# Optimization experiments

Measured on AMD Instinct MI355X. Metric: run time of the kernel, lower is better.

Reference implementation:

```python
import jax, jax.numpy as jnp
import numpy as np

H = 128
IN = 2048
PROJ = 64
EPS = 1e-5


def setup_inputs() -> dict:
    key = jax.random.key(0)
    ks = jax.random.split(key, 12)
    B, T = 64, 512
    s_in = 1.0 / np.sqrt(H)  # torch RNN init: U(-1/sqrt(H), 1/sqrt(H))
    u = lambda k, shape, s: jax.random.uniform(k, shape, jnp.float32, -s, s)
    return {
        "x": jax.random.normal(ks[0], (B, T, IN), jnp.float32),
        "W_ih1": u(ks[1], (H, IN), s_in),
        "W_hh1": u(ks[2], (H, H), s_in),
        "b_ih1": u(ks[3], (H,), s_in),
        "b_hh1": u(ks[4], (H,), s_in),
        "W_ih2": u(ks[5], (H, H), s_in),
        "W_hh2": u(ks[6], (H, H), s_in),
        "b_ih2": u(ks[7], (H,), s_in),
        "b_hh2": u(ks[8], (H,), s_in),
        "W_proj": u(ks[9], (PROJ, H), 1.0 / np.sqrt(H)),
        "b_proj": u(ks[10], (PROJ,), 1.0 / np.sqrt(H)),
        "gamma": jnp.ones((PROJ,), jnp.float32),
        "beta": jnp.zeros((PROJ,), jnp.float32),
    }


def _rnn(xproj, W_hh, collect):
    # xproj: [B, T, H] = x @ W_ih^T + b_ih + b_hh (biases folded in)
    B = xproj.shape[0]
    h0 = jnp.zeros((B, H), xproj.dtype)
    xs = jnp.swapaxes(xproj, 0, 1)  # [T, B, H]

    def step(h, xp):
        h = jnp.tanh(xp + h @ W_hh.T)
        return h, (h if collect else None)

    h_last, ys = jax.lax.scan(step, h0, xs)
    return h_last, (jnp.swapaxes(ys, 0, 1) if collect else None)


def reference(x, W_ih1, W_hh1, b_ih1, b_hh1, W_ih2, W_hh2, b_ih2, b_hh2,
              W_proj, b_proj, gamma, beta):
    # layer 1: hoist the big input GEMM out of the recurrence
    xp1 = jnp.einsum("bti,hi->bth", x, W_ih1) + (b_ih1 + b_hh1)
    _, y1 = _rnn(xp1, W_hh1, collect=True)  # [B, T, H]
    # layer 2: only final hidden state is needed
    xp2 = jnp.einsum("bth,gh->btg", y1, W_ih2) + (b_ih2 + b_hh2)
    h2, _ = _rnn(xp2, W_hh2, collect=False)  # [B, H]
    # projection + LayerNorm
    z = h2 @ W_proj.T + b_proj  # [B, 64]
    mu = jnp.mean(z, axis=-1, keepdims=True)
    var = jnp.mean((z - mu) ** 2, axis=-1, keepdims=True)
    return (z - mu) * jax.lax.rsqrt(var + EPS) * gamma + beta
```

## Files before the change

kernel.cpp:

```cpp
#include <hip/hip_runtime.h>
#include <math.h>

#define H 128
#define IN 2048
#define PROJ 64
#define BT 32768
#define T_STEPS 512
#define BATCH 64
#define BM 128
#define BKA 64

using f32x4  = __attribute__((ext_vector_type(4))) float;
using bfrag  = __attribute__((ext_vector_type(8))) short;
using h2_t   = __attribute__((ext_vector_type(2))) _Float16;

__device__ __forceinline__ unsigned cvtpk(float lo, float hi) {
  unsigned r;
  asm("v_cvt_pk_bf16_f32 %0, %1, %2" : "=v"(r) : "v"(lo), "v"(hi));
  return r;
}

__global__ __launch_bounds__(512) void xp1_gemm(
    const float* __restrict__ x, const float* __restrict__ W,
    const float* __restrict__ b1, const float* __restrict__ b2,
    float* __restrict__ xp1) {
  __shared__ __align__(16) char As[2][BM * BKA * 2];
  __shared__ __align__(16) char Bs[2][H * BKA * 2];
  const int t  = threadIdx.x;
  const int m0 = blockIdx.x * BM;
  const int wv = t >> 6, l = t & 63;
  const int wm = wv >> 2;
  const int wn = wv & 3;
  const int lr = l & 15;
  const int lq = l >> 4;

  const float* xg[4];
  const float* wg[4];
  int so[4];
#pragma unroll
  for (int i = 0; i < 4; ++i) {
    int c = t + 512 * i, r = c >> 4, k4 = c & 15;
    xg[i] = x + (size_t)(m0 + r) * IN + k4 * 4;
    wg[i] = W + (size_t)r * IN + k4 * 4;
    so[i] = (r * 128 + k4 * 8) ^ ((r & 7) << 4);
  }
  int ao[2][4], bo[2][2];
#pragma unroll
  for (int kf = 0; kf < 2; ++kf) {
#pragma unroll
    for (int mf = 0; mf < 4; ++mf) {
      int r = wm * 64 + mf * 16 + lr;
      ao[kf][mf] = (r * 128 + kf * 64 + lq * 16) ^ ((r & 7) << 4);
    }
#pragma unroll
    for (int nf = 0; nf < 2; ++nf) {
      int r = wn * 32 + nf * 16 + lr;
      bo[kf][nf] = (r * 128 + kf * 64 + lq * 16) ^ ((r & 7) << 4);
    }
  }

  f32x4 acc[4][2];
#pragma unroll
  for (int mf = 0; mf < 4; ++mf)
#pragma unroll
    for (int nf = 0; nf < 2; ++nf)
#pragma unroll
      for (int j = 0; j < 4; ++j) acc[mf][nf][j] = 0.f;

  float4 xr[4], wr[4];
#pragma unroll
  for (int i = 0; i < 4; ++i) {
    xr[i] = *(const float4*)&xg[i][0];
    wr[i] = *(const float4*)&wg[i][0];
  }
#pragma unroll
  for (int i = 0; i < 4; ++i) {
    uint2 ux; ux.x = cvtpk(xr[i].x, xr[i].y); ux.y = cvtpk(xr[i].z, xr[i].w);
    *(uint2*)(As[0] + so[i]) = ux;
    uint2 uw; uw.x = cvtpk(wr[i].x, wr[i].y); uw.y = cvtpk(wr[i].z, wr[i].w);
    *(uint2*)(Bs[0] + so[i]) = uw;
  }
  __syncthreads();

  for (int tc = 0; tc < 32; ++tc) {
    const int kc = (tc + 1) * BKA;
    if (tc < 31) {
#pragma unroll
      for (int i = 0; i < 4; ++i) {
        xr[i] = *(const float4*)&xg[i][kc];
        wr[i] = *(const float4*)&wg[i][kc];
      }
    }
    const char* Ab = As[tc & 1];
    const char* Bb = Bs[tc & 1];
#pragma unroll
    for (int kf = 0; kf < 2; ++kf) {
      bfrag af[4], bf[2];
#pragma unroll
      for (int mf = 0; mf < 4; ++mf) af[mf] = *(const bfrag*)(Ab + ao[kf][mf]);
#pragma unroll
      for (int nf = 0; nf < 2; ++nf) bf[nf] = *(const bfrag*)(Bb + bo[kf][nf]);
#pragma unroll
      for (int mf = 0; mf < 4; ++mf)
#pragma unroll
        for (int nf = 0; nf < 2; ++nf)
          acc[mf][nf] = __builtin_amdgcn_mfma_f32_16x16x32_bf16(
              af[mf], bf[nf], acc[mf][nf], 0, 0, 0);
    }
    if (tc < 31) {
      char* Aw = As[(tc + 1) & 1];
      char* Bw = Bs[(tc + 1) & 1];
#pragma unroll
      for (int i = 0; i < 4; ++i) {
        uint2 ux; ux.x = cvtpk(xr[i].x, xr[i].y); ux.y = cvtpk(xr[i].z, xr[i].w);
        *(uint2*)(Aw + so[i]) = ux;
        uint2 uw; uw.x = cvtpk(wr[i].x, wr[i].y); uw.y = cvtpk(wr[i].z, wr[i].w);
        *(uint2*)(Bw + so[i]) = uw;
      }
    }
    __syncthreads();
  }

#pragma unroll
  for (int nf = 0; nf < 2; ++nf) {
    int n = wn * 32 + nf * 16 + lr;
    float bias = b1[n] + b2[n];
#pragma unroll
    for (int mf = 0; mf < 4; ++mf) {
      int mr = m0 + wm * 64 + mf * 16 + lq * 4;
#pragma unroll
      for (int j = 0; j < 4; ++j)
        xp1[(size_t)(mr + j) * H + n] = acc[mf][nf][j] + bias;
    }
  }
}

struct Wrow { unsigned p0, p1, p2, p3, p4, p5, p6, p7; };

__device__ __forceinline__ float4 gload16(const float* p) {
  float4 r;
  asm volatile("global_load_dwordx4 %0, %1, off" : "=v"(r) : "v"(p));
  return r;
}

__device__ __forceinline__ unsigned pkh(float x, float y) {
  h2_t p = {(_Float16)x, (_Float16)y};
  return __builtin_bit_cast(unsigned, p);
}

__device__ __forceinline__ Wrow packrow(float4 a, float4 b, float4 c,
                                        float4 d) {
  Wrow w = {pkh(a.x, a.y), pkh(a.z, a.w), pkh(b.x, b.y), pkh(b.z, b.w),
            pkh(c.x, c.y), pkh(c.z, c.w), pkh(d.x, d.y), pkh(d.z, d.w)};
  return w;
}

__device__ __forceinline__ float d2(unsigned w, int h, float acc) {
  return __builtin_amdgcn_fdot2(__builtin_bit_cast(h2_t, w),
                                __builtin_bit_cast(h2_t, (unsigned)h), acc,
                                false);
}

__device__ __forceinline__ float dot16(Wrow w, int4 lo, int4 hi, float acc) {
  acc = d2(w.p0, lo.x, acc);
  acc = d2(w.p1, lo.y, acc);
  acc = d2(w.p2, lo.z, acc);
  acc = d2(w.p3, lo.w, acc);
  acc = d2(w.p4, hi.x, acc);
  acc = d2(w.p5, hi.y, acc);
  acc = d2(w.p6, hi.z, acc);
  acc = d2(w.p7, hi.w, acc);
  return acc;
}

template <int CTRL>
__device__ __forceinline__ float dpp_add(float x) {
  return x + __builtin_bit_cast(
                 float, __builtin_amdgcn_mov_dpp(__builtin_bit_cast(int, x),
                                                 CTRL, 0xf, 0xf, true));
}

__device__ __forceinline__ float red8(float v) {
  v = dpp_add<0xB1>(v);
  v = dpp_add<0x4E>(v);
  v = dpp_add<0x141>(v);
  return v;
}

__device__ __forceinline__ float fast_tanh(float x) {
  float e = __expf(2.0f * x);
  return 1.0f - 2.0f / (e + 1.0f);
}

__global__ __launch_bounds__(512)
__attribute__((amdgpu_waves_per_eu(1, 2)))
void rnn_fused(
    const float* __restrict__ xp1,
    const float* __restrict__ W_hh1, const float* __restrict__ W_ih2,
    const float* __restrict__ W_hh2, const float* __restrict__ b_ih2,
    const float* __restrict__ b_hh2, const float* __restrict__ W_proj,
    const float* __restrict__ b_proj, const float* __restrict__ gamma,
    const float* __restrict__ beta, float* __restrict__ out) {
  __shared__ __align__(16) _Float16 h1s[2][H];
  __shared__ __align__(16) _Float16 h2s[2][H];
  const int t = threadIdx.x;
  const int b = blockIdx.x;
  const int l = t & 63;
  const int w = t >> 6;
  const int g = (l >> 3) & 7;
  const int q = l & 7;
  const int r0 = 16 * w + g;
  const int r1 = r0 + 8;

  const float* pA = &W_hh1[r0 * H + 16 * q];
  const float* pB = &W_hh1[r1 * H + 16 * q];
  const float* pC = &W_ih2[r0 * H + 16 * q];
  const float* pD = &W_ih2[r1 * H + 16 * q];
  const float* pE = &W_hh2[r0 * H + 16 * q];
  const float* pF = &W_hh2[r1 * H + 16 * q];
  float4 A0 = gload16(pA), A1 = gload16(pA + 4), A2 = gload16(pA + 8), A3 = gload16(pA + 12);
  float4 B0 = gload16(pB), B1 = gload16(pB + 4), B2 = gload16(pB + 8), B3 = gload16(pB + 12);
  float4 C0 = gload16(pC), C1 = gload16(pC + 4), C2 = gload16(pC + 8), C3 = gload16(pC + 12);
  float4 D0 = gload16(pD), D1 = gload16(pD + 4), D2 = gload16(pD + 8), D3 = gload16(pD + 12);
  float4 E0 = gload16(pE), E1 = gload16(pE + 4), E2 = gload16(pE + 8), E3 = gload16(pE + 12);
  float4 F0 = gload16(pF), F1 = gload16(pF + 4), F2 = gload16(pF + 8), F3 = gload16(pF + 12);
  asm volatile("s_waitcnt vmcnt(0)" ::: "memory");

  Wrow W1r0 = packrow(A0, A1, A2, A3);
  Wrow W1r1 = packrow(B0, B1, B2, B3);
  Wrow W2r0 = packrow(C0, C1, C2, C3);
  Wrow W2r1 = packrow(D0, D1, D2, D3);
  Wrow W3r0 = packrow(E0, E1, E2, E3);
  Wrow W3r1 = packrow(F0, F1, F2, F3);

  const float bias2_0 = b_ih2[r0] + b_hh2[r0];
  const float bias2_1 = b_ih2[r1] + b_hh2[r1];

  if (t < H) { h1s[1][t] = (_Float16)0.f; h2s[1][t] = (_Float16)0.f; }
  __syncthreads();

  const float* xpr0 = xp1 + (size_t)b * T_STEPS * H + r0;
  const float* xpr1 = xpr0 + 8;

  if (q == 0) {
    h1s[0][r0] = (_Float16)fast_tanh(xpr0[0]);
    h1s[0][r1] = (_Float16)fast_tanh(xpr1[0]);
  }
  __syncthreads();

  float xpc0 = xpr0[H];
  float xpc1 = xpr1[H];

  for (int i = 1; i < T_STEPS; ++i) {
    const _Float16* h1p = h1s[(i - 1) & 1];
    const _Float16* h2p = h2s[i & 1];
    _Float16* h1w = h1s[i & 1];
    _Float16* h2w = h2s[(i - 1) & 1];

    float nx0 = 0.f, nx1 = 0.f;
    if (i + 1 < T_STEPS) {
      nx0 = xpr0[(size_t)(i + 1) * H];
      nx1 = xpr1[(size_t)(i + 1) * H];
    }

    int4 l1 = *(const int4*)&h1p[16 * q];
    int4 u1 = *(const int4*)&h1p[16 * q + 8];
    int4 l2 = *(const int4*)&h2p[16 * q];
    int4 u2 = *(const int4*)&h2p[16 * q + 8];

    float a0 = dot16(W1r0, l1, u1, 0.f);
    float a1 = dot16(W1r1, l1, u1, 0.f);
    float c0 = dot16(W3r0, l2, u2, 0.f);
    float c1 = dot16(W3r1, l2, u2, 0.f);
    float bb0 = dot16(W2r0, l1, u1, c0);
    float bb1 = dot16(W2r1, l1, u1, c1);

    a0 = red8(a0); a1 = red8(a1);
    bb0 = red8(bb0); bb1 = red8(bb1);

    float h1n0 = fast_tanh(xpc0 + a0);
    float h1n1 = fast_tanh(xpc1 + a1);
    float h2n0 = fast_tanh(bias2_0 + bb0);
    float h2n1 = fast_tanh(bias2_1 + bb1);
    if (q == 0) {
      h1w[r0] = (_Float16)h1n0; h1w[r1] = (_Float16)h1n1;
      h2w[r0] = (_Float16)h2n0; h2w[r1] = (_Float16)h2n1;
    }
    __syncthreads();
    xpc0 = nx0; xpc1 = nx1;
  }

  {
    const _Float16* h1p = h1s[(T_STEPS - 1) & 1];
    const _Float16* h2p = h2s[T_STEPS & 1];
    _Float16* h2w = h2s[(T_STEPS - 1) & 1];
    int4 l1 = *(const int4*)&h1p[16 * q];
    int4 u1 = *(const int4*)&h1p[16 * q + 8];
    int4 l2 = *(const int4*)&h2p[16 * q];
    int4 u2 = *(const int4*)&h2p[16 * q + 8];
    float c0 = dot16(W3r0, l2, u2, 0.f);
    float c1 = dot16(W3r1, l2, u2, 0.f);
    float bb0 = dot16(W2r0, l1, u1, c0);
    float bb1 = dot16(W2r1, l1, u1, c1);
    bb0 = red8(bb0); bb1 = red8(bb1);
    if (q == 0) {
      h2w[r0] = (_Float16)fast_tanh(bias2_0 + bb0);
      h2w[r1] = (_Float16)fast_tanh(bias2_1 + bb1);
    }
    __syncthreads();
  }

  if (t < PROJ) {
    const float* wp = W_proj + t * H;
    float z = b_proj[t];
#pragma unroll
    for (int i = 0; i < 32; ++i) {
      float4 wv = *(const float4*)&wp[4 * i];
      z = fmaf(wv.x, (float)h2s[1][4 * i + 0], z);
      z = fmaf(wv.y, (float)h2s[1][4 * i + 1], z);
      z = fmaf(wv.z, (float)h2s[1][4 * i + 2], z);
      z = fmaf(wv.w, (float)h2s[1][4 * i + 3], z);
    }
    float s = z;
#pragma unroll
    for (int d = 1; d < 64; d <<= 1) s += __shfl_xor(s, d);
    float mu = s * 0.015625f;
    float dz = z - mu;
    float v = dz * dz;
#pragma unroll
    for (int d = 1; d < 64; d <<= 1) v += __shfl_xor(v, d);
    float rstd = rsqrtf(v * 0.015625f + 1e-5f);
    out[b * PROJ + t] = dz * rstd * gamma[t] + beta[t];
  }
}

extern "C" void kernel_launch(void* const* d_in, const int* in_sizes, int n_in,
                              void* d_out, int out_size, void* d_ws, size_t ws_size,
                              hipStream_t stream) {
  const float* x      = (const float*)d_in[0];
  const float* W_ih1  = (const float*)d_in[1];
  const float* W_hh1  = (const float*)d_in[2];
  const float* b_ih1  = (const float*)d_in[3];
  const float* b_hh1  = (const float*)d_in[4];
  const float* W_ih2  = (const float*)d_in[5];
  const float* W_hh2  = (const float*)d_in[6];
  const float* b_ih2  = (const float*)d_in[7];
  const float* b_hh2  = (const float*)d_in[8];
  const float* W_proj = (const float*)d_in[9];
  const float* b_proj = (const float*)d_in[10];
  const float* gamma  = (const float*)d_in[11];
  const float* beta   = (const float*)d_in[12];

  float* xp1 = (float*)d_ws;

  xp1_gemm<<<BT / BM, 512, 0, stream>>>(x, W_ih1, b_ih1, b_hh1, xp1);
  rnn_fused<<<BATCH, 512, 0, stream>>>(xp1, W_hh1, W_ih2, W_hh2, b_ih2, b_hh2,
                                       W_proj, b_proj, gamma, beta,
                                       (float*)d_out);
}
```

Measured before the change: 409.9 us.

## Halve recurrence block to 256 threads with four rows per lane group

The fused RNN kernel now runs 4 waves per block instead of 8. Each lane group owns four hidden rows instead of two, so it holds 12 packed fp16 weight rows in registers. The goal is cheaper per-step __syncthreads and fewer waves contending, at the cost of twice as many dot products per thread on the serial recurrence path and higher register pressure. The weight loads now use an asm helper that waits after each row, which serializes the one-time prologue loads. The final projection still uses t < PROJ, so it needs 64 threads, which 256 covers.

```diff
diff --git a/kernel.cpp b/kernel.cpp
--- a/kernel.cpp
+++ b/kernel.cpp
@@ -137,12 +137,6 @@
 
 struct Wrow { unsigned p0, p1, p2, p3, p4, p5, p6, p7; };
 
-__device__ __forceinline__ float4 gload16(const float* p) {
-  float4 r;
-  asm volatile("global_load_dwordx4 %0, %1, off" : "=v"(r) : "v"(p));
-  return r;
-}
-
 __device__ __forceinline__ unsigned pkh(float x, float y) {
   h2_t p = {(_Float16)x, (_Float16)y};
   return __builtin_bit_cast(unsigned, p);
@@ -153,6 +147,21 @@
   Wrow w = {pkh(a.x, a.y), pkh(a.z, a.w), pkh(b.x, b.y), pkh(b.z, b.w),
             pkh(c.x, c.y), pkh(c.z, c.w), pkh(d.x, d.y), pkh(d.z, d.w)};
   return w;
+}
+
+__device__ __forceinline__ Wrow loadrow_safe(const float* p) {
+  float4 a, b, c, d;
+  asm volatile(
+      "global_load_dwordx4 %0, %4, off\n\t"
+      "global_load_dwordx4 %1, %5, off\n\t"
+      "global_load_dwordx4 %2, %6, off\n\t"
+      "global_load_dwordx4 %3, %7, off\n\t"
+      "s_waitcnt vmcnt(0)"
+      : "=&v"(a), "=&v"(b), "=&v"(c), "=&v"(d)
+      : "v"(p), "v"(p + 4), "v"(p + 8), "v"(p + 12)
+      : "memory");
+  __builtin_amdgcn_sched_barrier(0);
+  return packrow(a, b, c, d);
 }
 
 __device__ __forceinline__ float d2(unsigned w, int h, float acc) {
@@ -192,8 +201,8 @@
   return 1.0f - 2.0f / (e + 1.0f);
 }
 
-__global__ __launch_bounds__(512)
-__attribute__((amdgpu_waves_per_eu(1, 2)))
+__global__ __launch_bounds__(256)
+__attribute__((amdgpu_waves_per_eu(1, 1)))
 void rnn_fused(
     const float* __restrict__ xp1,
     const float* __restrict__ W_hh1, const float* __restrict__ W_ih2,
@@ -209,47 +218,40 @@
   const int w = t >> 6;
   const int g = (l >> 3) & 7;
   const int q = l & 7;
-  const int r0 = 16 * w + g;
-  const int r1 = r0 + 8;
-
-  const float* pA = &W_hh1[r0 * H + 16 * q];
-  const float* pB = &W_hh1[r1 * H + 16 * q];
-  const float* pC = &W_ih2[r0 * H + 16 * q];
-  const float* pD = &W_ih2[r1 * H + 16 * q];
-  const float* pE = &W_hh2[r0 * H + 16 * q];
-  const float* pF = &W_hh2[r1 * H + 16 * q];
-  float4 A0 = gload16(pA), A1 = gload16(pA + 4), A2 = gload16(pA + 8), A3 = gload16(pA + 12);
-  float4 B0 = gload16(pB), B1 = gload16(pB + 4), B2 = gload16(pB + 8), B3 = gload16(pB + 12);
-  float4 C0 = gload16(pC), C1 = gload16(pC + 4), C2 = gload16(pC + 8), C3 = gload16(pC + 12);
-  float4 D0 = gload16(pD), D1 = gload16(pD + 4), D2 = gload16(pD + 8), D3 = gload16(pD + 12);
-  float4 E0 = gload16(pE), E1 = gload16(pE + 4), E2 = gload16(pE + 8), E3 = gload16(pE + 12);
-  float4 F0 = gload16(pF), F1 = gload16(pF + 4), F2 = gload16(pF + 8), F3 = gload16(pF + 12);
-  asm volatile("s_waitcnt vmcnt(0)" ::: "memory");
-
-  Wrow W1r0 = packrow(A0, A1, A2, A3);
-  Wrow W1r1 = packrow(B0, B1, B2, B3);
-  Wrow W2r0 = packrow(C0, C1, C2, C3);
-  Wrow W2r1 = packrow(D0, D1, D2, D3);
-  Wrow W3r0 = packrow(E0, E1, E2, E3);
-  Wrow W3r1 = packrow(F0, F1, F2, F3);
-
-  const float bias2_0 = b_ih2[r0] + b_hh2[r0];
-  const float bias2_1 = b_ih2[r1] + b_hh2[r1];
+
+  Wrow W1[4], W2[4], W3[4];
+  float bias2[4];
+  const float* xpr[4];
+#pragma unroll
+  for (int m = 0; m < 4; ++m) {
+    const int r = 32 * w + g + 8 * m;
+    W1[m] = loadrow_safe(&W_hh1[r * H + 16 * q]);
+    W2[m] = loadrow_safe(&W_ih2[r * H + 16 * q]);
+    W3[m] = loadrow_safe(&W_hh2[r * H + 16 * q]);
+    bias2[m] = b_ih2[r] + b_hh2[r];
+    xpr[m] = xpr[0];
+  }
+#pragma unroll
+  for (int m = 0; m < 4; ++m) {
+    const int r = 32 * w + g + 8 * m;
+    xpr[m] = xp1 + (size_t)b * T_STEPS * H + r;
+  }
 
   if (t < H) { h1s[1][t] = (_Float16)0.f; h2s[1][t] = (_Float16)0.f; }
   __syncthreads();
 
-  const float* xpr0 = xp1 + (size_t)b * T_STEPS * H + r0;
-  const float* xpr1 = xpr0 + 8;
-
   if (q == 0) {
-    h1s[0][r0] = (_Float16)fast_tanh(xpr0[0]);
-    h1s[0][r1] = (_Float16)fast_tanh(xpr1[0]);
+#pragma unroll
+    for (int m = 0; m < 4; ++m) {
+      const int r = 32 * w + g + 8 * m;
+      h1s[0][r] = (_Float16)fast_tanh(xpr[m][0]);
+    }
   }
   __syncthreads();
 
-  float xpc0 = xpr0[H];
-  float xpc1 = xpr1[H];
+  float xpc[4];
+#pragma unroll
+  for (int m = 0; m < 4; ++m) xpc[m] = xpr[m][H];
 
   for (int i = 1; i < T_STEPS; ++i) {
     const _Float16* h1p = h1s[(i - 1) & 1];
@@ -257,37 +259,37 @@
     _Float16* h1w = h1s[i & 1];
     _Float16* h2w = h2s[(i - 1) & 1];
 
-    float nx0 = 0.f, nx1 = 0.f;
-    if (i + 1 < T_STEPS) {
-      nx0 = xpr0[(size_t)(i + 1) * H];
-      nx1 = xpr1[(size_t)(i + 1) * H];
-    }
+    float nx[4];
+#pragma unroll
+    for (int m = 0; m < 4; ++m)
+      nx[m] = (i + 1 < T_STEPS) ? xpr[m][(size_t)(i + 1) * H] : 0.f;
 
     int4 l1 = *(const int4*)&h1p[16 * q];
     int4 u1 = *(const int4*)&h1p[16 * q + 8];
     int4 l2 = *(const int4*)&h2p[16 * q];
     int4 u2 = *(const int4*)&h2p[16 * q + 8];
 
-    float a0 = dot16(W1r0, l1, u1, 0.f);
-    float a1 = dot16(W1r1, l1, u1, 0.f);
-    float c0 = dot16(W3r0, l2, u2, 0.f);
-    float c1 = dot16(W3r1, l2, u2, 0.f);
-    float bb0 = dot16(W2r0, l1, u1, c0);
-    float bb1 = dot16(W2r1, l1, u1, c1);
-
-    a0 = red8(a0); a1 = red8(a1);
-    bb0 = red8(bb0); bb1 = red8(bb1);
-
-    float h1n0 = fast_tanh(xpc0 + a0);
-    float h1n1 = fast_tanh(xpc1 + a1);
-    float h2n0 = fast_tanh(bias2_0 + bb0);
-    float h2n1 = fast_tanh(bias2_1 + bb1);
+    float a[4], bb[4];
+#pragma unroll
+    for (int m = 0; m < 4; ++m) {
+      a[m] = dot16(W1[m], l1, u1, 0.f);
+      float c = dot16(W3[m], l2, u2, 0.f);
+      bb[m] = dot16(W2[m], l1, u1, c);
+    }
+#pragma unroll
+    for (int m = 0; m < 4; ++m) { a[m] = red8(a[m]); bb[m] = red8(bb[m]); }
+
     if (q == 0) {
-      h1w[r0] = (_Float16)h1n0; h1w[r1] = (_Float16)h1n1;
-      h2w[r0] = (_Float16)h2n0; h2w[r1] = (_Float16)h2n1;
+#pragma unroll
+      for (int m = 0; m < 4; ++m) {
+        const int r = 32 * w + g + 8 * m;
+        h1w[r] = (_Float16)fast_tanh(xpc[m] + a[m]);
+        h2w[r] = (_Float16)fast_tanh(bias2[m] + bb[m]);
+      }
     }
     __syncthreads();
-    xpc0 = nx0; xpc1 = nx1;
+#pragma unroll
+    for (int m = 0; m < 4; ++m) xpc[m] = nx[m];
   }
 
   {
@@ -298,14 +300,19 @@
     int4 u1 = *(const int4*)&h1p[16 * q + 8];
     int4 l2 = *(const int4*)&h2p[16 * q];
     int4 u2 = *(const int4*)&h2p[16 * q + 8];
-    float c0 = dot16(W3r0, l2, u2, 0.f);
-    float c1 = dot16(W3r1, l2, u2, 0.f);
-    float bb0 = dot16(W2r0, l1, u1, c0);
-    float bb1 = dot16(W2r1, l1, u1, c1);
-    bb0 = red8(bb0); bb1 = red8(bb1);
+    float bb[4];
+#pragma unroll
+    for (int m = 0; m < 4; ++m) {
+      float c = dot16(W3[m], l2, u2, 0.f);
+      bb[m] = dot16(W2[m], l1, u1, c);
+      bb[m] = red8(bb[m]);
+    }
     if (q == 0) {
-      h2w[r0] = (_Float16)fast_tanh(bias2_0 + bb0);
-      h2w[r1] = (_Float16)fast_tanh(bias2_1 + bb1);
+#pragma unroll
+      for (int m = 0; m < 4; ++m) {
+        const int r = 32 * w + g + 8 * m;
+        h2w[r] = (_Float16)fast_tanh(bias2[m] + bb[m]);
+      }
     }
     __syncthreads();
   }
@@ -354,7 +361,7 @@
   float* xp1 = (float*)d_ws;
 
   xp1_gemm<<<BT / BM, 512, 0, stream>>>(x, W_ih1, b_ih1, b_hh1, xp1);
-  rnn_fused<<<BATCH, 512, 0, stream>>>(xp1, W_hh1, W_ih2, W_hh2, b_ih2, b_hh2,
+  rnn_fused<<<BATCH, 256, 0, stream>>>(xp1, W_hh1, W_ih2, W_hh2, b_ih2, b_hh2,
                                        W_proj, b_proj, gamma, beta,
                                        (float*)d_out);
 }
```

Result: slower. 431.8 us (+5.3%).

## Stage xp1 chunks into double-buffered LDS and use lightweight barriers

Applied to the files above, without the earlier changes.

Replaces the per-step global loads of the layer-1 input projection with bulk loads of 64-timestep chunks into a double-buffered shared-memory buffer. Each chunk is prefetched into registers one chunk ahead and written to LDS at the chunk boundary. __syncthreads is swapped for an explicit lgkmcnt wait plus s_barrier, which trims the per-step synchronization cost. The cost is 64KB of LDS and a vmcnt wait every 64 steps. Global loads issued inside the loop may also make the lgkmcnt-only barrier interact with outstanding vm loads.

```diff
diff --git a/kernel.cpp b/kernel.cpp
--- a/kernel.cpp
+++ b/kernel.cpp
@@ -9,6 +9,7 @@
 #define BATCH 64
 #define BM 128
 #define BKA 64
+#define CH 64
 
 using f32x4  = __attribute__((ext_vector_type(4))) float;
 using bfrag  = __attribute__((ext_vector_type(8))) short;
@@ -137,10 +138,19 @@
 
 struct Wrow { unsigned p0, p1, p2, p3, p4, p5, p6, p7; };
 
-__device__ __forceinline__ float4 gload16(const float* p) {
+__device__ __forceinline__ float4 gld(const float* p) {
   float4 r;
   asm volatile("global_load_dwordx4 %0, %1, off" : "=v"(r) : "v"(p));
   return r;
+}
+
+__device__ __forceinline__ void waitv0() {
+  asm volatile("s_waitcnt vmcnt(0)" ::: "memory");
+  __builtin_amdgcn_sched_barrier(0);
+}
+
+__device__ __forceinline__ void bar() {
+  asm volatile("s_waitcnt lgkmcnt(0)\n\ts_barrier" ::: "memory");
 }
 
 __device__ __forceinline__ unsigned pkh(float x, float y) {
@@ -201,6 +211,7 @@
     const float* __restrict__ b_hh2, const float* __restrict__ W_proj,
     const float* __restrict__ b_proj, const float* __restrict__ gamma,
     const float* __restrict__ beta, float* __restrict__ out) {
+  __shared__ float xbuf[2][CH * H];
   __shared__ __align__(16) _Float16 h1s[2][H];
   __shared__ __align__(16) _Float16 h2s[2][H];
   const int t = threadIdx.x;
@@ -218,13 +229,13 @@
   const float* pD = &W_ih2[r1 * H + 16 * q];
   const float* pE = &W_hh2[r0 * H + 16 * q];
   const float* pF = &W_hh2[r1 * H + 16 * q];
-  float4 A0 = gload16(pA), A1 = gload16(pA + 4), A2 = gload16(pA + 8), A3 = gload16(pA + 12);
-  float4 B0 = gload16(pB), B1 = gload16(pB + 4), B2 = gload16(pB + 8), B3 = gload16(pB + 12);
-  float4 C0 = gload16(pC), C1 = gload16(pC + 4), C2 = gload16(pC + 8), C3 = gload16(pC + 12);
-  float4 D0 = gload16(pD), D1 = gload16(pD + 4), D2 = gload16(pD + 8), D3 = gload16(pD + 12);
-  float4 E0 = gload16(pE), E1 = gload16(pE + 4), E2 = gload16(pE + 8), E3 = gload16(pE + 12);
-  float4 F0 = gload16(pF), F1 = gload16(pF + 4), F2 = gload16(pF + 8), F3 = gload16(pF + 12);
-  asm volatile("s_waitcnt vmcnt(0)" ::: "memory");
+  float4 A0 = gld(pA), A1 = gld(pA + 4), A2 = gld(pA + 8), A3 = gld(pA + 12);
+  float4 B0 = gld(pB), B1 = gld(pB + 4), B2 = gld(pB + 8), B3 = gld(pB + 12);
+  float4 C0 = gld(pC), C1 = gld(pC + 4), C2 = gld(pC + 8), C3 = gld(pC + 12);
+  float4 D0 = gld(pD), D1 = gld(pD + 4), D2 = gld(pD + 8), D3 = gld(pD + 12);
+  float4 E0 = gld(pE), E1 = gld(pE + 4), E2 = gld(pE + 8), E3 = gld(pE + 12);
+  float4 F0 = gld(pF), F1 = gld(pF + 4), F2 = gld(pF + 8), F3 = gld(pF + 12);
+  waitv0();
 
   Wrow W1r0 = packrow(A0, A1, A2, A3);
   Wrow W1r1 = packrow(B0, B1, B2, B3);
@@ -236,37 +247,57 @@
   const float bias2_0 = b_ih2[r0] + b_hh2[r0];
   const float bias2_1 = b_ih2[r1] + b_hh2[r1];
 
+  const float* xpB = xp1 + (size_t)b * T_STEPS * H;
+
+  float4 xs0 = gld(xpB + 0 * 2048 + 4 * t);
+  float4 xs1 = gld(xpB + 1 * 2048 + 4 * t);
+  float4 xs2 = gld(xpB + 2 * 2048 + 4 * t);
+  float4 xs3 = gld(xpB + 3 * 2048 + 4 * t);
+  waitv0();
+  *(float4*)&xbuf[0][0 * 2048 + 4 * t] = xs0;
+  *(float4*)&xbuf[0][1 * 2048 + 4 * t] = xs1;
+  *(float4*)&xbuf[0][2 * 2048 + 4 * t] = xs2;
+  *(float4*)&xbuf[0][3 * 2048 + 4 * t] = xs3;
   if (t < H) { h1s[1][t] = (_Float16)0.f; h2s[1][t] = (_Float16)0.f; }
-  __syncthreads();
-
-  const float* xpr0 = xp1 + (size_t)b * T_STEPS * H + r0;
-  const float* xpr1 = xpr0 + 8;
+  bar();
 
   if (q == 0) {
-    h1s[0][r0] = (_Float16)fast_tanh(xpr0[0]);
-    h1s[0][r1] = (_Float16)fast_tanh(xpr1[0]);
-  }
-  __syncthreads();
-
-  float xpc0 = xpr0[H];
-  float xpc1 = xpr1[H];
-
+    h1s[0][r0] = (_Float16)fast_tanh(xbuf[0][r0]);
+    h1s[0][r1] = (_Float16)fast_tanh(xbuf[0][r1]);
+  }
+  {
+    const float* gp = xpB + CH * H;
+    xs0 = gld(gp + 0 * 2048 + 4 * t);
+    xs1 = gld(gp + 1 * 2048 + 4 * t);
+    xs2 = gld(gp + 2 * 2048 + 4 * t);
+    xs3 = gld(gp + 3 * 2048 + 4 * t);
+  }
+  bar();
+
+#pragma unroll 1
   for (int i = 1; i < T_STEPS; ++i) {
+    const int c  = i >> 6;
+    const int ic = i & 63;
+    const float* xcur = xbuf[c & 1];
     const _Float16* h1p = h1s[(i - 1) & 1];
     const _Float16* h2p = h2s[i & 1];
     _Float16* h1w = h1s[i & 1];
     _Float16* h2w = h2s[(i - 1) & 1];
 
-    float nx0 = 0.f, nx1 = 0.f;
-    if (i + 1 < T_STEPS) {
-      nx0 = xpr0[(size_t)(i + 1) * H];
-      nx1 = xpr1[(size_t)(i + 1) * H];
+    if (ic == 0 && c >= 1 && c < 7) {
+      const float* gp = xpB + (size_t)(c + 1) * CH * H;
+      xs0 = gld(gp + 0 * 2048 + 4 * t);
+      xs1 = gld(gp + 1 * 2048 + 4 * t);
+      xs2 = gld(gp + 2 * 2048 + 4 * t);
+      xs3 = gld(gp + 3 * 2048 + 4 * t);
     }
 
     int4 l1 = *(const int4*)&h1p[16 * q];
     int4 u1 = *(const int4*)&h1p[16 * q + 8];
     int4 l2 = *(const int4*)&h2p[16 * q];
     int4 u2 = *(const int4*)&h2p[16 * q + 8];
+    float xv0 = xcur[ic * H + r0];
+    float xv1 = xcur[ic * H + r1];
 
     float a0 = dot16(W1r0, l1, u1, 0.f);
     float a1 = dot16(W1r1, l1, u1, 0.f);
@@ -278,16 +309,22 @@
     a0 = red8(a0); a1 = red8(a1);
     bb0 = red8(bb0); bb1 = red8(bb1);
 
-    float h1n0 = fast_tanh(xpc0 + a0);
-    float h1n1 = fast_tanh(xpc1 + a1);
-    float h2n0 = fast_tanh(bias2_0 + bb0);
-    float h2n1 = fast_tanh(bias2_1 + bb1);
     if (q == 0) {
-      h1w[r0] = (_Float16)h1n0; h1w[r1] = (_Float16)h1n1;
-      h2w[r0] = (_Float16)h2n0; h2w[r1] = (_Float16)h2n1;
-    }
-    __syncthreads();
-    xpc0 = nx0; xpc1 = nx1;
+      h1w[r0] = (_Float16)fast_tanh(xv0 + a0);
+      h1w[r1] = (_Float16)fast_tanh(xv1 + a1);
+      h2w[r0] = (_Float16)fast_tanh(bias2_0 + bb0);
+      h2w[r1] = (_Float16)fast_tanh(bias2_1 + bb1);
+    }
+
+    if (ic == 63 && c < 7) {
+      waitv0();
+      float* dst = xbuf[(c + 1) & 1];
+      *(float4*)&dst[0 * 2048 + 4 * t] = xs0;
+      *(float4*)&dst[1 * 2048 + 4 * t] = xs1;
+      *(float4*)&dst[2 * 2048 + 4 * t] = xs2;
+      *(float4*)&dst[3 * 2048 + 4 * t] = xs3;
+    }
+    bar();
   }
 
   {
@@ -307,7 +344,7 @@
       h2w[r0] = (_Float16)fast_tanh(bias2_0 + bb0);
       h2w[r1] = (_Float16)fast_tanh(bias2_1 + bb1);
     }
-    __syncthreads();
+    bar();
   }
 
   if (t < PROJ) {
```

After: 435.4 us. 1.06x slower.

## Pair adjacent rows per lane, prefetch xp two steps ahead, use lightweight barrier

Applied to the files above, without the earlier changes.

Each lane group now owns two adjacent hidden rows instead of rows eight apart. This allows float2 loads of the input projection and packed 32-bit fp16 stores of the new hidden state. The xp prefetch distance grows from one step to two, and the recurrence loop is unrolled by two with compile-time buffer parity. __syncthreads is replaced by an explicit lgkmcnt wait plus s_barrier, which avoids waiting on outstanding global loads. Together these aim to cut per-step latency on the serial recurrence path, at the risk of ordering issues from the hand-written barrier.

```diff
diff --git a/kernel.cpp b/kernel.cpp
--- a/kernel.cpp
+++ b/kernel.cpp
@@ -137,10 +137,19 @@
 
 struct Wrow { unsigned p0, p1, p2, p3, p4, p5, p6, p7; };
 
-__device__ __forceinline__ float4 gload16(const float* p) {
+__device__ __forceinline__ float4 gld(const float* p) {
   float4 r;
   asm volatile("global_load_dwordx4 %0, %1, off" : "=v"(r) : "v"(p));
   return r;
+}
+
+__device__ __forceinline__ void waitv0() {
+  asm volatile("s_waitcnt vmcnt(0)" ::: "memory");
+  __builtin_amdgcn_sched_barrier(0);
+}
+
+__device__ __forceinline__ void bar() {
+  asm volatile("s_waitcnt lgkmcnt(0)\n\ts_barrier" ::: "memory");
 }
 
 __device__ __forceinline__ unsigned pkh(float x, float y) {
@@ -209,8 +218,8 @@
   const int w = t >> 6;
   const int g = (l >> 3) & 7;
   const int q = l & 7;
-  const int r0 = 16 * w + g;
-  const int r1 = r0 + 8;
+  const int r0 = 16 * w + 2 * g;
+  const int r1 = r0 + 1;
 
   const float* pA = &W_hh1[r0 * H + 16 * q];
   const float* pB = &W_hh1[r1 * H + 16 * q];
@@ -218,13 +227,13 @@
   const float* pD = &W_ih2[r1 * H + 16 * q];
   const float* pE = &W_hh2[r0 * H + 16 * q];
   const float* pF = &W_hh2[r1 * H + 16 * q];
-  float4 A0 = gload16(pA), A1 = gload16(pA + 4), A2 = gload16(pA + 8), A3 = gload16(pA + 12);
-  float4 B0 = gload16(pB), B1 = gload16(pB + 4), B2 = gload16(pB + 8), B3 = gload16(pB + 12);
-  float4 C0 = gload16(pC), C1 = gload16(pC + 4), C2 = gload16(pC + 8), C3 = gload16(pC + 12);
-  float4 D0 = gload16(pD), D1 = gload16(pD + 4), D2 = gload16(pD + 8), D3 = gload16(pD + 12);
-  float4 E0 = gload16(pE), E1 = gload16(pE + 4), E2 = gload16(pE + 8), E3 = gload16(pE + 12);
-  float4 F0 = gload16(pF), F1 = gload16(pF + 4), F2 = gload16(pF + 8), F3 = gload16(pF + 12);
-  asm volatile("s_waitcnt vmcnt(0)" ::: "memory");
+  float4 A0 = gld(pA), A1 = gld(pA + 4), A2 = gld(pA + 8), A3 = gld(pA + 12);
+  float4 B0 = gld(pB), B1 = gld(pB + 4), B2 = gld(pB + 8), B3 = gld(pB + 12);
+  float4 C0 = gld(pC), C1 = gld(pC + 4), C2 = gld(pC + 8), C3 = gld(pC + 12);
+  float4 D0 = gld(pD), D1 = gld(pD + 4), D2 = gld(pD + 8), D3 = gld(pD + 12);
+  float4 E0 = gld(pE), E1 = gld(pE + 4), E2 = gld(pE + 8), E3 = gld(pE + 12);
+  float4 F0 = gld(pF), F1 = gld(pF + 4), F2 = gld(pF + 8), F3 = gld(pF + 12);
+  waitv0();
 
   Wrow W1r0 = packrow(A0, A1, A2, A3);
   Wrow W1r1 = packrow(B0, B1, B2, B3);
@@ -239,61 +248,59 @@
   if (t < H) { h1s[1][t] = (_Float16)0.f; h2s[1][t] = (_Float16)0.f; }
   __syncthreads();
 
-  const float* xpr0 = xp1 + (size_t)b * T_STEPS * H + r0;
-  const float* xpr1 = xpr0 + 8;
+  const float* xpr = xp1 + (size_t)b * T_STEPS * H + r0;
 
   if (q == 0) {
-    h1s[0][r0] = (_Float16)fast_tanh(xpr0[0]);
-    h1s[0][r1] = (_Float16)fast_tanh(xpr1[0]);
+    float2 x0 = *(const float2*)&xpr[0];
+    *(unsigned*)&h1s[0][r0] = pkh(fast_tanh(x0.x), fast_tanh(x0.y));
   }
   __syncthreads();
 
-  float xpc0 = xpr0[H];
-  float xpc1 = xpr1[H];
-
-  for (int i = 1; i < T_STEPS; ++i) {
-    const _Float16* h1p = h1s[(i - 1) & 1];
-    const _Float16* h2p = h2s[i & 1];
-    _Float16* h1w = h1s[i & 1];
-    _Float16* h2w = h2s[(i - 1) & 1];
-
-    float nx0 = 0.f, nx1 = 0.f;
-    if (i + 1 < T_STEPS) {
-      nx0 = xpr0[(size_t)(i + 1) * H];
-      nx1 = xpr1[(size_t)(i + 1) * H];
-    }
-
-    int4 l1 = *(const int4*)&h1p[16 * q];
-    int4 u1 = *(const int4*)&h1p[16 * q + 8];
-    int4 l2 = *(const int4*)&h2p[16 * q];
-    int4 u2 = *(const int4*)&h2p[16 * q + 8];
-
-    float a0 = dot16(W1r0, l1, u1, 0.f);
-    float a1 = dot16(W1r1, l1, u1, 0.f);
-    float c0 = dot16(W3r0, l2, u2, 0.f);
-    float c1 = dot16(W3r1, l2, u2, 0.f);
-    float bb0 = dot16(W2r0, l1, u1, c0);
-    float bb1 = dot16(W2r1, l1, u1, c1);
-
-    a0 = red8(a0); a1 = red8(a1);
-    bb0 = red8(bb0); bb1 = red8(bb1);
-
-    float h1n0 = fast_tanh(xpc0 + a0);
-    float h1n1 = fast_tanh(xpc1 + a1);
-    float h2n0 = fast_tanh(bias2_0 + bb0);
-    float h2n1 = fast_tanh(bias2_1 + bb1);
-    if (q == 0) {
-      h1w[r0] = (_Float16)h1n0; h1w[r1] = (_Float16)h1n1;
-      h2w[r0] = (_Float16)h2n0; h2w[r1] = (_Float16)h2n1;
-    }
-    __syncthreads();
-    xpc0 = nx0; xpc1 = nx1;
-  }
+  float2 xc = *(const float2*)&xpr[1 * H];
+  float2 xn = *(const float2*)&xpr[2 * H];
+
+#define STEP(I, PAR)                                                         \
+  {                                                                          \
+    const _Float16* h1p = h1s[(PAR) ^ 1];                       \
+    const _Float16* h2p = h2s[(PAR)];                           \
+    _Float16* h1w = h1s[(PAR)];                                 \
+    _Float16* h2w = h2s[(PAR) ^ 1];                             \
+    float2 xf = float2{0.f, 0.f};                                            \
+    if ((I) + 2 < T_STEPS) xf = *(const float2*)&xpr[(size_t)((I) + 2) * H]; \
+    int4 l1 = *(const int4*)&h1p[16 * q];                                    \
+    int4 u1 = *(const int4*)&h1p[16 * q + 8];                                \
+    int4 l2 = *(const int4*)&h2p[16 * q];                                    \
+    int4 u2 = *(const int4*)&h2p[16 * q + 8];                                \
+    float a0 = dot16(W1r0, l1, u1, 0.f);                                     \
+    float a1 = dot16(W1r1, l1, u1, 0.f);                                     \
+    float c0 = dot16(W3r0, l2, u2, 0.f);                                     \
+    float c1 = dot16(W3r1, l2, u2, 0.f);                                     \
+    float bb0 = dot16(W2r0, l1, u1, c0);                                     \
+    float bb1 = dot16(W2r1, l1, u1, c1);                                     \
+    a0 = red8(a0); a1 = red8(a1);                                            \
+    bb0 = red8(bb0); bb1 = red8(bb1);                                        \
+    if (q == 0) {                                                            \
+      *(unsigned*)&h1w[r0] =                                                 \
+          pkh(fast_tanh(xc.x + a0), fast_tanh(xc.y + a1));                   \
+      *(unsigned*)&h2w[r0] =                                                 \
+          pkh(fast_tanh(bias2_0 + bb0), fast_tanh(bias2_1 + bb1));           \
+    }                                                                        \
+    bar();                                                                   \
+    xc = xn; xn = xf;                                                        \
+  }
+
+  STEP(1, 1)
+#pragma unroll 1
+  for (int i = 2; i < T_STEPS; i += 2) {
+    STEP(i, 0)
+    STEP(i + 1, 1)
+  }
+#undef STEP
 
   {
-    const _Float16* h1p = h1s[(T_STEPS - 1) & 1];
-    const _Float16* h2p = h2s[T_STEPS & 1];
-    _Float16* h2w = h2s[(T_STEPS - 1) & 1];
+    const _Float16* h1p = h1s[1];
+    const _Float16* h2p = h2s[0];
+    _Float16* h2w = h2s[1];
     int4 l1 = *(const int4*)&h1p[16 * q];
     int4 u1 = *(const int4*)&h1p[16 * q + 8];
     int4 l2 = *(const int4*)&h2p[16 * q];
@@ -304,10 +311,10 @@
     float bb1 = dot16(W2r1, l1, u1, c1);
     bb0 = red8(bb0); bb1 = red8(bb1);
     if (q == 0) {
-      h2w[r0] = (_Float16)fast_tanh(bias2_0 + bb0);
-      h2w[r1] = (_Float16)fast_tanh(bias2_1 + bb1);
-    }
-    __syncthreads();
+      *(unsigned*)&h2w[r0] =
+          pkh(fast_tanh(bias2_0 + bb0), fast_tanh(bias2_1 + bb1));
+    }
+    bar();
   }
 
   if (t < PROJ) {
```

New measurement: 397.3 us, median of 2. 1.03x faster.
